# Optimization experiments

Measured on AMD Instinct MI355X. Metric: run time of the kernel, lower is better.

The kernel has to match this reference:

```python
import jax, jax.numpy as jnp
import numpy as np

B, Q, S1, S2 = 4, 256, 2048, 2048   # batch, latents, kv lengths
D, H, K, F = 2048, 16, 128, 8192    # embed_dim, heads, key_size, ffn dim
LN_EPS = 1e-5


def _layer_norm(x, scale, offset):
    mu = jnp.mean(x, axis=-1, keepdims=True)
    var = jnp.var(x, axis=-1, keepdims=True)
    return (x - mu) * jax.lax.rsqrt(var + LN_EPS) * scale + offset


def _cross_attention(q_in, kv_in, wq, bq, wk, bk, wv, bv, wo, bo, bias_k, bias_v):
    b, q_len, _ = q_in.shape
    t = kv_in.shape[1]
    qh = (q_in @ wq + bq).reshape(b, q_len, H, K)
    kh = (kv_in @ wk + bk).reshape(b, t, H, K)
    vh = (kv_in @ wv + bv).reshape(b, t, H, K)
    # ESM-style learned bias key/value appended as one extra kv position
    kh = jnp.concatenate([kh, jnp.broadcast_to(bias_k, (b, 1, H, K))], axis=1)
    vh = jnp.concatenate([vh, jnp.broadcast_to(bias_v, (b, 1, H, K))], axis=1)
    scale = jnp.sqrt(jnp.asarray(K, q_in.dtype))
    logits = jnp.einsum('bqhk,bthk->bhqt', qh, kh) / scale  # [B,H,Q,T+1]
    weights = jax.nn.softmax(logits, axis=-1)
    ctx = jnp.einsum('bhqt,bthk->bqhk', weights, vh).reshape(b, q_len, H * K)
    return ctx @ wo + bo


def _forward(x, xf_1, xf_2,
             ln1_scale, ln1_offset, wq1, bq1, wk1, bk1, wv1, bv1, wo1, bo1, bias_k1, bias_v1,
             ln2_scale, ln2_offset, wq2, bq2, wk2, bk2, wv2, bv2, wo2, bo2, bias_k2, bias_v2,
             ln_mlp_scale, ln_mlp_offset, w_fc1, b_fc1, w_fc2, b_fc2):
    res = x
    h = _layer_norm(x, ln1_scale, ln1_offset)
    x = res + _cross_attention(h, xf_1, wq1, bq1, wk1, bk1, wv1, bv1, wo1, bo1, bias_k1, bias_v1)
    res = x
    h = _layer_norm(x, ln2_scale, ln2_offset)
    x = res + _cross_attention(h, xf_2, wq2, bq2, wk2, bk2, wv2, bv2, wo2, bo2, bias_k2, bias_v2)
    h = _layer_norm(x, ln_mlp_scale, ln_mlp_offset)
    h = jax.nn.gelu(h @ w_fc1 + b_fc1, approximate=False) @ w_fc2 + b_fc2
    return x + h


def setup_inputs() -> dict:
    key = jax.random.key(0)
    ks = iter(jax.random.split(key, 64))

    def rn(shape, s=0.02):
        return jax.random.normal(next(ks), shape, jnp.float32) * s

    inp = {
        'x': rn((B, Q, D), 1.0),
        'xf_1': rn((B, S1, D), 1.0),
        'xf_2': rn((B, S2, D), 1.0),
    }
    for i in (1, 2):
        inp[f'ln{i}_scale'] = jnp.ones((D,), jnp.float32)
        inp[f'ln{i}_offset'] = jnp.zeros((D,), jnp.float32)
        inp[f'wq{i}'] = rn((D, H * K))
        inp[f'bq{i}'] = jnp.zeros((H * K,), jnp.float32)
        inp[f'wk{i}'] = rn((D, H * K))
        inp[f'bk{i}'] = jnp.zeros((H * K,), jnp.float32)
        inp[f'wv{i}'] = rn((D, H * K))
        inp[f'bv{i}'] = jnp.zeros((H * K,), jnp.float32)
        inp[f'wo{i}'] = rn((H * K, D))
        inp[f'bo{i}'] = jnp.zeros((D,), jnp.float32)
        inp[f'bias_k{i}'] = rn((1, 1, H, K))
        inp[f'bias_v{i}'] = rn((1, 1, H, K))
    inp['ln_mlp_scale'] = jnp.ones((D,), jnp.float32)
    inp['ln_mlp_offset'] = jnp.zeros((D,), jnp.float32)
    inp['w_fc1'] = rn((D, F))
    inp['b_fc1'] = jnp.zeros((F,), jnp.float32)
    inp['w_fc2'] = rn((F, D))
    inp['b_fc2'] = jnp.zeros((D,), jnp.float32)
    return inp


def reference(x, xf_1, xf_2,
              ln1_scale, ln1_offset, wq1, bq1, wk1, bk1, wv1, bv1, wo1, bo1, bias_k1, bias_v1,
              ln2_scale, ln2_offset, wq2, bq2, wk2, bk2, wv2, bv2, wo2, bo2, bias_k2, bias_v2,
              ln_mlp_scale, ln_mlp_offset, w_fc1, b_fc1, w_fc2, b_fc2):
    return _forward(x, xf_1, xf_2,
                    ln1_scale, ln1_offset, wq1, bq1, wk1, bk1, wv1, bv1, wo1, bo1, bias_k1, bias_v1,
                    ln2_scale, ln2_offset, wq2, bq2, wk2, bk2, wv2, bv2, wo2, bo2, bias_k2, bias_v2,
                    ln_mlp_scale, ln_mlp_offset, w_fc1, b_fc1, w_fc2, b_fc2)
```

## Files before the change

kernel.cpp:

```cpp
#include <hip/hip_runtime.h>

typedef __attribute__((ext_vector_type(8))) short bf16x8;
typedef __attribute__((ext_vector_type(4))) float f32x4;

#define D_EMB 2048
#define NQ    256
#define NB    4
#define NS    2048
#define NH    16
#define HK    128
#define FF    8192

__device__ __forceinline__ float b2f(short s) {
  union { unsigned int u; float f; } c;
  c.u = ((unsigned int)(unsigned short)s) << 16;
  return c.f;
}
__device__ __forceinline__ short f2b(float f) {
  union { float f; unsigned int u; } c; c.f = f;
  unsigned int u = c.u;
  u += 0x7FFFu + ((u >> 16) & 1u);
  return (short)(u >> 16);
}
__device__ __forceinline__ void gload_lds16(const short* g, short* l) {
  __builtin_amdgcn_global_load_lds(
      (const __attribute__((address_space(1))) void*)g,
      (__attribute__((address_space(3))) void*)l, 16, 0, 0);
}

__global__ __launch_bounds__(256)
void cvt_kernel(const float* __restrict__ in, short* __restrict__ out, int n8) {
  const int i = (blockIdx.x * 256 + threadIdx.x) * 8;
  if (i >= n8) return;
  f32x4 a = *(const f32x4*)(in + i), b = *(const f32x4*)(in + i + 4);
  bf16x8 t;
#pragma unroll
  for (int j = 0; j < 4; ++j) { t[j] = f2b(a[j]); t[4 + j] = f2b(b[j]); }
  *(bf16x8*)(out + i) = t;
}

__global__ __launch_bounds__(256)
void transpose_kernel(const float* __restrict__ W, short* __restrict__ Wt,
                      int Kd, int N) {
  __shared__ short tile[64][65];
  const int k0 = blockIdx.y * 64, n0 = blockIdx.x * 64;
  const int tid = threadIdx.x;
  const int r = tid >> 2, c4 = (tid & 3) * 16;
#pragma unroll
  for (int i = 0; i < 16; i += 4) {
    f32x4 v = *(const f32x4*)(W + (size_t)(k0 + r) * N + n0 + c4 + i);
#pragma unroll
    for (int j = 0; j < 4; ++j) tile[c4 + i + j][r] = f2b(v[j]);
  }
  __syncthreads();
  bf16x8 o0, o1;
#pragma unroll
  for (int j = 0; j < 8; ++j) { o0[j] = tile[r][c4 + j]; o1[j] = tile[r][c4 + 8 + j]; }
  short* dst = Wt + (size_t)(n0 + r) * Kd + k0 + c4;
  *(bf16x8*)dst = o0;
  *(bf16x8*)(dst + 8) = o1;
}

__global__ __launch_bounds__(256)
void ln_kernel(const float* __restrict__ x, const float* __restrict__ scale,
               const float* __restrict__ offset, short* __restrict__ out) {
  const int row = blockIdx.x, tid = threadIdx.x;
  const float* xr = x + (size_t)row * D_EMB + tid * 8;
  f32x4 v0 = *(const f32x4*)xr;
  f32x4 v1 = *(const f32x4*)(xr + 4);
  float f[8], s = 0.f, sq = 0.f;
#pragma unroll
  for (int i = 0; i < 4; ++i) { f[i] = v0[i]; f[4 + i] = v1[i]; }
#pragma unroll
  for (int i = 0; i < 8; ++i) { s += f[i]; sq += f[i] * f[i]; }
#pragma unroll
  for (int off = 1; off < 64; off <<= 1) {
    s  += __shfl_xor(s, off, 64);
    sq += __shfl_xor(sq, off, 64);
  }
  __shared__ float red[2][4];
  const int w = tid >> 6;
  if ((tid & 63) == 0) { red[0][w] = s; red[1][w] = sq; }
  __syncthreads();
  s  = red[0][0] + red[0][1] + red[0][2] + red[0][3];
  sq = red[1][0] + red[1][1] + red[1][2] + red[1][3];
  const float mu  = s * (1.f / D_EMB);
  const float var = sq * (1.f / D_EMB) - mu * mu;
  const float inv = rsqrtf(var + 1e-5f);
  bf16x8 ov;
#pragma unroll
  for (int i = 0; i < 8; ++i) {
    const int c = tid * 8 + i;
    ov[i] = f2b((f[i] - mu) * inv * scale[c] + offset[c]);
  }
  *(bf16x8*)(out + (size_t)row * D_EMB + tid * 8) = ov;
}

template<int EPI, int OUTF>
__global__ __launch_bounds__(256)
void gemm_kernel(const short* __restrict__ A, const short* __restrict__ Bt,
                 const float* __restrict__ bias, const float* __restrict__ res,
                 void* __restrict__ Cp, int M, int N, int Kd) {
  __shared__ short ldsA[128 * 32];
  __shared__ short ldsB[128 * 32];
  const int tid = threadIdx.x;
  const int m0 = blockIdx.y * 128, n0 = blockIdx.x * 128;
  const int w = tid >> 6, lane = tid & 63, l15 = lane & 15, quad = lane >> 4;
  const int wr = (w >> 1) * 64, wc = (w & 1) * 64;
  const int sr = tid >> 2;
  const int sc = (tid & 3) * 8;
  f32x4 acc[4][4];
#pragma unroll
  for (int mi = 0; mi < 4; ++mi)
#pragma unroll
    for (int ni = 0; ni < 4; ++ni) acc[mi][ni] = (f32x4){0.f, 0.f, 0.f, 0.f};

  const short* pa0 = A  + (size_t)(m0 + sr) * Kd + sc;
  const short* pa1 = A  + (size_t)(m0 + 64 + sr) * Kd + sc;
  const short* pb0 = Bt + (size_t)(n0 + sr) * Kd + sc;
  const short* pb1 = Bt + (size_t)(n0 + 64 + sr) * Kd + sc;

  for (int k0 = 0; k0 < Kd; k0 += 32) {
    __syncthreads();
    gload_lds16(pa0 + k0, ldsA + tid * 8);
    gload_lds16(pa1 + k0, ldsA + 2048 + tid * 8);
    gload_lds16(pb0 + k0, ldsB + tid * 8);
    gload_lds16(pb1 + k0, ldsB + 2048 + tid * 8);
    __syncthreads();
    bf16x8 af[4], bfr[4];
#pragma unroll
    for (int mi = 0; mi < 4; ++mi)
      af[mi] = *(bf16x8*)&ldsA[(wr + mi * 16 + l15) * 32 + quad * 8];
#pragma unroll
    for (int ni = 0; ni < 4; ++ni)
      bfr[ni] = *(bf16x8*)&ldsB[(wc + ni * 16 + l15) * 32 + quad * 8];
#pragma unroll
    for (int mi = 0; mi < 4; ++mi)
#pragma unroll
      for (int ni = 0; ni < 4; ++ni)
        acc[mi][ni] = __builtin_amdgcn_mfma_f32_16x16x32_bf16(
            af[mi], bfr[ni], acc[mi][ni], 0, 0, 0);
  }

#pragma unroll
  for (int mi = 0; mi < 4; ++mi) {
#pragma unroll
    for (int ni = 0; ni < 4; ++ni) {
      const int gn = n0 + wc + ni * 16 + l15;
      const float bv = bias[gn];
#pragma unroll
      for (int r = 0; r < 4; ++r) {
        const int gm = m0 + wr + mi * 16 + quad * 4 + r;
        float v = acc[mi][ni][r] + bv;
        if (EPI == 1) v += res[(size_t)gm * N + gn];
        if (EPI == 2) v = 0.5f * v * (1.f + erff(v * 0.70710678118654752f));
        if (OUTF) ((float*)Cp)[(size_t)gm * N + gn] = v;
        else      ((short*)Cp)[(size_t)gm * N + gn] = f2b(v);
      }
    }
  }
}

#define FENCE() asm volatile("" ::: "memory")

#define G_STAGE(DB2, DSTOFF, PS0, PS1, KON)                                     \
  gload_lds16((PS0) + (KON), sh + (DB2) * 32768 + (DSTOFF) + tid * 8);          \
  gload_lds16((PS1) + (KON), sh + (DB2) * 32768 + (DSTOFF) + 4096 + tid * 8);

#define PHASE(DB, MG, KH, DSTOFF, PS0, PS1, KON, DOVM)                          \
  {                                                                             \
    const short* _ra = sh + (DB) * 32768 + (KH) * 8192;                         \
    const short* _rb = sh + (DB) * 32768 + 16384 + (KH) * 8192;                 \
    if ((MG) == 0) {                                                            \
      bfrag[0] = *(const bf16x8*)(_rb + boff[0]);                               \
      bfrag[1] = *(const bf16x8*)(_rb + boff[1]);                               \
      bfrag[2] = *(const bf16x8*)(_rb + boff[2]);                               \
      bfrag[3] = *(const bf16x8*)(_rb + boff[3]);                               \
    }                                                                           \
    afrag[0] = *(const bf16x8*)(_ra + aoff[(MG) * 4 + 0]);                      \
    afrag[1] = *(const bf16x8*)(_ra + aoff[(MG) * 4 + 1]);                      \
    afrag[2] = *(const bf16x8*)(_ra + aoff[(MG) * 4 + 2]);                      \
    afrag[3] = *(const bf16x8*)(_ra + aoff[(MG) * 4 + 3]);                      \
    G_STAGE((DB) ^ 1, DSTOFF, PS0, PS1, KON)                                    \
    if (DOVM) asm volatile("s_waitcnt vmcnt(4)" ::: "memory");                  \
    __builtin_amdgcn_s_barrier();                                               \
    FENCE();                                                                    \
    __builtin_amdgcn_s_setprio(1);                                              \
    _Pragma("unroll")                                                           \
    for (int mf = 0; mf < 4; ++mf)                                              \
      _Pragma("unroll")                                                         \
      for (int nf = 0; nf < 4; ++nf)                                            \
        acc[(MG) * 4 + mf][nf] = __builtin_amdgcn_mfma_f32_16x16x32_bf16(       \
            afrag[mf], bfrag[nf], acc[(MG) * 4 + mf][nf], 0, 0, 0);             \
    __builtin_amdgcn_s_setprio(0);                                              \
    __builtin_amdgcn_s_barrier();                                               \
    FENCE();                                                                    \
  }

#define TILE(DB, KON)                                                           \
  PHASE(DB, 0, 0, 0,     pA0, pA1, (KON), 0)                                    \
  PHASE(DB, 1, 0, 16384, pB0, pB1, (KON), 1)                                    \
  PHASE(DB, 0, 1, 8192,  pA0, pA1, (KON) + 32, 0)                               \
  PHASE(DB, 1, 1, 24576, pB0, pB1, (KON) + 32, 1)

template<int EPI, int OUTF>
__global__ __launch_bounds__(512, 2)
void gemm256_kernel(const short* __restrict__ A, const short* __restrict__ Bt,
                    const float* __restrict__ bias, const float* __restrict__ res,
                    void* __restrict__ Cp, int M, int N, int Kd) {
  __shared__ short sh[65536];
  const int tid = threadIdx.x;
  const int w = tid >> 6, lane = tid & 63;
  const int l15 = lane & 15, quad = lane >> 4;
  const int wm = w >> 2, wn = w & 3;

  const int nTn = N >> 8;
  const int cpx = gridDim.x >> 3;
  const int wid = (blockIdx.x & 7) * cpx + (blockIdx.x >> 3);
  const int m0 = (wid / nTn) * 256, n0 = (wid % nTn) * 256;

  const int c0 = tid, c1 = 512 + tid;
  const int r0 = ((c0 >> 5) << 3) + (c0 & 7), kb0 = (c0 >> 3) & 3;
  const int r1 = ((c1 >> 5) << 3) + (c1 & 7), kb1 = (c1 >> 3) & 3;
  const short* pA0 = A  + (size_t)(m0 + r0) * Kd + kb0 * 8;
  const short* pA1 = A  + (size_t)(m0 + r1) * Kd + kb1 * 8;
  const short* pB0 = Bt + (size_t)(n0 + r0) * Kd + kb0 * 8;
  const short* pB1 = Bt + (size_t)(n0 + r1) * Kd + kb1 * 8;

  int aoff[8], boff[4];
#pragma unroll
  for (int mf = 0; mf < 8; ++mf) {
    const int r = wm * 128 + mf * 16 + l15;
    aoff[mf] = ((r >> 3) << 8) + (quad << 6) + ((r & 7) << 3);
  }
#pragma unroll
  for (int nf = 0; nf < 4; ++nf) {
    const int r = wn * 64 + nf * 16 + l15;
    boff[nf] = ((r >> 3) << 8) + (quad << 6) + ((r & 7) << 3);
  }

  f32x4 acc[8][4];
#pragma unroll
  for (int mf = 0; mf < 8; ++mf)
#pragma unroll
    for (int nf = 0; nf < 4; ++nf) acc[mf][nf] = (f32x4){0.f, 0.f, 0.f, 0.f};
  bf16x8 afrag[4], bfrag[4];

  const int NT = Kd >> 6;

  G_STAGE(0, 0,     pA0, pA1, 0)
  G_STAGE(0, 16384, pB0, pB1, 0)
  G_STAGE(0, 8192,  pA0, pA1, 32)
  G_STAGE(0, 24576, pB0, pB1, 32)
  asm volatile("s_waitcnt vmcnt(4)" ::: "memory");
  __builtin_amdgcn_s_barrier();
  FENCE();

  for (int kt = 0; kt < NT; kt += 2) {
    const int k1n = (kt + 1) * 64;
    const int k2n = (kt + 2 < NT) ? (kt + 2) * 64 : 0;
    TILE(0, k1n)
    TILE(1, k2n)
  }
  asm volatile("s_waitcnt vmcnt(0) lgkmcnt(0)" ::: "memory");

#pragma unroll
  for (int mf = 0; mf < 8; ++mf) {
#pragma unroll
    for (int nf = 0; nf < 4; ++nf) {
      const int gn = n0 + wn * 64 + nf * 16 + l15;
      const float bv = bias[gn];
#pragma unroll
      for (int r = 0; r < 4; ++r) {
        const int gm = m0 + wm * 128 + mf * 16 + quad * 4 + r;
        float v = acc[mf][nf][r] + bv;
        if (EPI == 1) v += res[(size_t)gm * N + gn];
        if (EPI == 2) v = 0.5f * v * (1.f + erff(v * 0.70710678118654752f));
        if (OUTF) ((float*)Cp)[(size_t)gm * N + gn] = v;
        else      ((short*)Cp)[(size_t)gm * N + gn] = f2b(v);
      }
    }
  }
}

__global__ __launch_bounds__(256)
void attn_part_kernel(const short* __restrict__ qh, const short* __restrict__ kh,
                      const short* __restrict__ vh, float* __restrict__ po,
                      float* __restrict__ pml) {
  const int bx = blockIdx.x;
  const int work = (bx & 7) * 128 + (bx >> 3);
  const int bh = work >> 4, sub = work & 15;
  const int qt = sub >> 2, split = sub & 3;
  const int b = bh >> 4, h = bh & 15;
  const int tid = threadIdx.x, w = tid >> 6, lane = tid & 63;
  const int l15 = lane & 15, quad = lane >> 4;
  const int q0 = qt * 64 + w * 16;

  __shared__ short ldsK[32 * 128];
  __shared__ short ldsV[128 * 32];
  __shared__ short ldsP[4 * 16 * 32];

  const float sc = 0.08838834764831845f;

  bf16x8 aq[4];
  {
    const short* qrow = qh + ((size_t)(b * 256 + q0 + l15)) * D_EMB + h * 128;
#pragma unroll
    for (int s = 0; s < 4; ++s)
      aq[s] = *(const bf16x8*)(qrow + s * 32 + quad * 8);
  }

  f32x4 o[8];
  float m_run[4], l_run[4];
#pragma unroll
  for (int dt = 0; dt < 8; ++dt) o[dt] = (f32x4){0.f, 0.f, 0.f, 0.f};
#pragma unroll
  for (int r = 0; r < 4; ++r) { m_run[r] = -INFINITY; l_run[r] = 0.f; }

  const int srow = tid >> 4;
  const int j = tid & 15;
  const int ksw = (j ^ (srow & 7)) * 8;
  const int t_beg = split * 512;

  for (int t0 = t_beg; t0 < t_beg + 512; t0 += 32) {
    __syncthreads();
    const size_t kb0 = ((size_t)(b * NS + t0 + srow)) * D_EMB + h * 128;
    const size_t kb1 = kb0 + (size_t)16 * D_EMB;
    gload_lds16(kh + kb0 + ksw, ldsK + tid * 8);
    gload_lds16(kh + kb1 + ksw, ldsK + 2048 + tid * 8);
    {
      bf16x8 v0 = *(const bf16x8*)(vh + kb0 + j * 8);
      bf16x8 v1 = *(const bf16x8*)(vh + kb1 + j * 8);
#pragma unroll
      for (int i = 0; i < 8; ++i) {
        const int d = j * 8 + i;
        const int swz = ((d >> 3) & 3) << 4;
        char* base = (char*)ldsV + (d << 6);
        *(short*)(base + ((srow << 1) ^ swz))        = v0[i];
        *(short*)(base + (((srow + 16) << 1) ^ swz)) = v1[i];
      }
    }
    __syncthreads();

    f32x4 s0 = (f32x4){0.f, 0.f, 0.f, 0.f}, s1 = (f32x4){0.f, 0.f, 0.f, 0.f};
    const int kswr = (l15 & 7) << 4;
#pragma unroll
    for (int s = 0; s < 4; ++s) {
      const int cb = s * 64 + quad * 16;
      bf16x8 k0f = *(bf16x8*)((char*)ldsK + (l15 << 8)        + (cb ^ kswr));
      bf16x8 k1f = *(bf16x8*)((char*)ldsK + ((16 + l15) << 8) + (cb ^ kswr));
      s0 = __builtin_amdgcn_mfma_f32_16x16x32_bf16(aq[s], k0f, s0, 0, 0, 0);
      s1 = __builtin_amdgcn_mfma_f32_16x16x32_bf16(aq[s], k1f, s1, 0, 0, 0);
    }

    float alpha_r[4];
#pragma unroll
    for (int r = 0; r < 4; ++r) {
      const float v0 = s0[r] * sc, v1 = s1[r] * sc;
      float mx = fmaxf(v0, v1);
#pragma unroll
      for (int off = 1; off < 16; off <<= 1) mx = fmaxf(mx, __shfl_xor(mx, off, 16));
      const float m_new = fmaxf(m_run[r], mx);
      const float p0 = expf(v0 - m_new), p1 = expf(v1 - m_new);
      float rs = p0 + p1;
#pragma unroll
      for (int off = 1; off < 16; off <<= 1) rs += __shfl_xor(rs, off, 16);
      alpha_r[r] = expf(m_run[r] - m_new);
      l_run[r] = l_run[r] * alpha_r[r] + rs;
      m_run[r] = m_new;
      const int prow = quad * 4 + r;
      const int psw = ((prow >> 1) & 3) << 4;
      char* pb = (char*)ldsP + w * 1024 + (prow << 6);
      *(short*)(pb + ((l15 << 1) ^ psw))        = f2b(p0);
      *(short*)(pb + (((16 + l15) << 1) ^ psw)) = f2b(p1);
    }
#pragma unroll
    for (int dt = 0; dt < 8; ++dt)
#pragma unroll
      for (int r = 0; r < 4; ++r) o[dt][r] *= alpha_r[r];

    bf16x8 pf = *(bf16x8*)((char*)ldsP + w * 1024 + (l15 << 6) +
                           ((quad << 4) ^ (((l15 >> 1) & 3) << 4)));
#pragma unroll
    for (int dt = 0; dt < 8; ++dt) {
      const int drow = dt * 16 + l15;
      bf16x8 vf = *(bf16x8*)((char*)ldsV + (drow << 6) +
                             ((quad << 4) ^ (((drow >> 3) & 3) << 4)));
      o[dt] = __builtin_amdgcn_mfma_f32_16x16x32_bf16(pf, vf, o[dt], 0, 0, 0);
    }
  }

  const int orow_base = (bh * 4 + qt) * 64 + w * 16;
#pragma unroll
  for (int dt = 0; dt < 8; ++dt)
#pragma unroll
    for (int r = 0; r < 4; ++r) {
      const size_t orow = (size_t)(orow_base + quad * 4 + r);
      po[(orow * 4 + split) * 128 + dt * 16 + l15] = o[dt][r];
    }
  if (l15 == 0) {
#pragma unroll
    for (int r = 0; r < 4; ++r) {
      const size_t orow = (size_t)(orow_base + quad * 4 + r);
      pml[(orow * 4 + split) * 2]     = m_run[r];
      pml[(orow * 4 + split) * 2 + 1] = l_run[r];
    }
  }
}

__global__ __launch_bounds__(256)
void attn_combine_kernel(const short* __restrict__ qh, const float* __restrict__ bias_k,
                         const float* __restrict__ bias_v, const float* __restrict__ po,
                         const float* __restrict__ pml, short* __restrict__ ctx) {
  const int tid = threadIdx.x, w = tid >> 6, lane = tid & 63;
  const int task = blockIdx.x * 4 + w;
  const int bh = task >> 8, qr = task & 255;
  const int b = bh >> 4, h = bh & 15;
  const int d0 = lane * 2;
  const float sc = 0.08838834764831845f;

  const short* qrow = qh + ((size_t)(b * 256 + qr)) * D_EMB + h * 128 + d0;
  const unsigned int qv = *(const unsigned int*)qrow;
  const float q0 = b2f((short)(qv & 0xffffu));
  const float q1 = b2f((short)(qv >> 16));
  const float2 bk = *(const float2*)(bias_k + h * 128 + d0);
  float le = q0 * bk.x + q1 * bk.y;
#pragma unroll
  for (int off = 1; off < 64; off <<= 1) le += __shfl_xor(le, off, 64);
  le *= sc;

  const float* pm = pml + (size_t)task * 8;
  float m[4], l[4];
#pragma unroll
  for (int s = 0; s < 4; ++s) { m[s] = pm[s * 2]; l[s] = pm[s * 2 + 1]; }
  float mt = le;
#pragma unroll
  for (int s = 0; s < 4; ++s) mt = fmaxf(mt, m[s]);

  const float pe = expf(le - mt);
  const float2 bv = *(const float2*)(bias_v + h * 128 + d0);
  float acc0 = pe * bv.x, acc1 = pe * bv.y;
  float lt = pe;
#pragma unroll
  for (int s = 0; s < 4; ++s) {
    const float es = expf(m[s] - mt);
    lt += l[s] * es;
    const float2 op = *(const float2*)(po + ((size_t)task * 4 + s) * 128 + d0);
    acc0 += es * op.x;
    acc1 += es * op.y;
  }
  const float inv = 1.f / lt;
  const unsigned int pack =
      ((unsigned int)(unsigned short)f2b(acc1 * inv) << 16) |
      (unsigned short)f2b(acc0 * inv);
  *(unsigned int*)(ctx + ((size_t)(b * 256 + qr)) * D_EMB + h * 128 + d0) = pack;
}

extern "C" void kernel_launch(void* const* d_in, const int* in_sizes, int n_in,
                              void* d_out, int out_size, void* d_ws, size_t ws_size,
                              hipStream_t stream) {
  const float* x   = (const float*)d_in[0];
  const float* xf1 = (const float*)d_in[1];
  const float* xf2 = (const float*)d_in[2];
  const float* L1[12]; const float* L2[12];
  for (int j = 0; j < 12; ++j) { L1[j] = (const float*)d_in[3 + j]; L2[j] = (const float*)d_in[15 + j]; }
  const float* ln_mlp_s = (const float*)d_in[27];
  const float* ln_mlp_o = (const float*)d_in[28];
  const float* w_fc1    = (const float*)d_in[29];
  const float* b_fc1    = (const float*)d_in[30];
  const float* w_fc2    = (const float*)d_in[31];
  const float* b_fc2    = (const float*)d_in[32];
  float* out = (float*)d_out;

  const size_t SZ_XQ  = (size_t)NB * NQ * D_EMB;
  const size_t SZ_KV  = (size_t)NB * NS * D_EMB;
  const size_t SZ_W   = (size_t)FF * D_EMB;

  float* x1   = (float*)d_ws;
  float* x2   = x1 + SZ_XQ;
  short* h_ln = (short*)(x2 + SZ_XQ);
  short* qh   = h_ln + SZ_XQ;
  short* ctxb = qh + SZ_XQ;
  short* kh   = ctxb + SZ_XQ;
  short* vh   = kh + SZ_KV;
  short* xfb  = vh + SZ_KV;
  short* Wt   = xfb + SZ_KV;
  short* fc1b = kh;
  float* po   = (float*)Wt;
  float* pml  = (float*)h_ln;

  const dim3 blk(256);
  const dim3 blk5(512);
  const dim3 g_q(D_EMB / 128, (NB * NQ) / 128);
  const dim3 g_kv256((NB * NS / 256) * (D_EMB / 256));
  const dim3 g_f1(FF / 128, (NB * NQ) / 128);
  const dim3 g_tw(D_EMB / 64, D_EMB / 64);
  const dim3 g_tf1(FF / 64, D_EMB / 64);
  const dim3 g_tf2(D_EMB / 64, FF / 64);
  const int  g_cvt = (int)(SZ_KV / 8 / 256);

  cvt_kernel<<<g_cvt, blk, 0, stream>>>(xf1, xfb, (int)SZ_KV);
  ln_kernel<<<NB * NQ, blk, 0, stream>>>(x, L1[0], L1[1], h_ln);
  transpose_kernel<<<g_tw, blk, 0, stream>>>(L1[2], Wt, D_EMB, D_EMB);
  gemm_kernel<0,0><<<g_q,  blk, 0, stream>>>(h_ln, Wt, L1[3], nullptr, qh, NB * NQ, D_EMB, D_EMB);
  transpose_kernel<<<g_tw, blk, 0, stream>>>(L1[4], Wt, D_EMB, D_EMB);
  gemm256_kernel<0,0><<<g_kv256, blk5, 0, stream>>>(xfb, Wt, L1[5], nullptr, kh, NB * NS, D_EMB, D_EMB);
  transpose_kernel<<<g_tw, blk, 0, stream>>>(L1[6], Wt, D_EMB, D_EMB);
  gemm256_kernel<0,0><<<g_kv256, blk5, 0, stream>>>(xfb, Wt, L1[7], nullptr, vh, NB * NS, D_EMB, D_EMB);
  attn_part_kernel<<<1024, blk, 0, stream>>>(qh, kh, vh, po, pml);
  attn_combine_kernel<<<4096, blk, 0, stream>>>(qh, L1[10], L1[11], po, pml, ctxb);
  transpose_kernel<<<g_tw, blk, 0, stream>>>(L1[8], Wt, D_EMB, D_EMB);
  gemm_kernel<1,1><<<g_q,  blk, 0, stream>>>(ctxb, Wt, L1[9], x, x1, NB * NQ, D_EMB, D_EMB);

  cvt_kernel<<<g_cvt, blk, 0, stream>>>(xf2, xfb, (int)SZ_KV);
  ln_kernel<<<NB * NQ, blk, 0, stream>>>(x1, L2[0], L2[1], h_ln);
  transpose_kernel<<<g_tw, blk, 0, stream>>>(L2[2], Wt, D_EMB, D_EMB);
  gemm_kernel<0,0><<<g_q,  blk, 0, stream>>>(h_ln, Wt, L2[3], nullptr, qh, NB * NQ, D_EMB, D_EMB);
  transpose_kernel<<<g_tw, blk, 0, stream>>>(L2[4], Wt, D_EMB, D_EMB);
  gemm256_kernel<0,0><<<g_kv256, blk5, 0, stream>>>(xfb, Wt, L2[5], nullptr, kh, NB * NS, D_EMB, D_EMB);
  transpose_kernel<<<g_tw, blk, 0, stream>>>(L2[6], Wt, D_EMB, D_EMB);
  gemm256_kernel<0,0><<<g_kv256, blk5, 0, stream>>>(xfb, Wt, L2[7], nullptr, vh, NB * NS, D_EMB, D_EMB);
  attn_part_kernel<<<1024, blk, 0, stream>>>(qh, kh, vh, po, pml);
  attn_combine_kernel<<<4096, blk, 0, stream>>>(qh, L2[10], L2[11], po, pml, ctxb);
  transpose_kernel<<<g_tw, blk, 0, stream>>>(L2[8], Wt, D_EMB, D_EMB);
  gemm_kernel<1,1><<<g_q,  blk, 0, stream>>>(ctxb, Wt, L2[9], x1, x2, NB * NQ, D_EMB, D_EMB);

  ln_kernel<<<NB * NQ, blk, 0, stream>>>(x2, ln_mlp_s, ln_mlp_o, h_ln);
  transpose_kernel<<<g_tf1, blk, 0, stream>>>(w_fc1, Wt, D_EMB, FF);
  gemm_kernel<2,0><<<g_f1, blk, 0, stream>>>(h_ln, Wt, b_fc1, nullptr, fc1b, NB * NQ, FF, D_EMB);
  transpose_kernel<<<g_tf2, blk, 0, stream>>>(w_fc2, Wt, FF, D_EMB);
  gemm_kernel<1,1><<<g_q,  blk, 0, stream>>>(fc1b, Wt, b_fc2, x2, out, NB * NQ, D_EMB, FF);
}
```

Measured before the change: 1.299 ms.

## Replace small-M GEMMs with split-K 256-tile kernel plus combine epilogue

Adds a split-K mode to the 256x256 pipelined GEMM kernel. It is used for the Q, output and FC projections, where M=1024 gave the old 128-tile kernel too few blocks to fill the GPU. Each split writes fp32 partials into reused workspace (the K/V buffers). A new vectorized combine kernel then sums the partials and applies bias, residual or GELU. The trade is more CU parallelism and a stronger inner loop against large extra partial-sum traffic (tens of MB per GEMM) and one extra launch per GEMM.

```diff
diff --git a/kernel.cpp b/kernel.cpp
--- a/kernel.cpp
+++ b/kernel.cpp
@@ -1,6 +1,7 @@
 #include <hip/hip_runtime.h>
 
 typedef __attribute__((ext_vector_type(8))) short bf16x8;
+typedef __attribute__((ext_vector_type(4))) short short4v;
 typedef __attribute__((ext_vector_type(4))) float f32x4;
 
 #define D_EMB 2048
@@ -94,71 +95,6 @@
     ov[i] = f2b((f[i] - mu) * inv * scale[c] + offset[c]);
   }
   *(bf16x8*)(out + (size_t)row * D_EMB + tid * 8) = ov;
-}
-
-template<int EPI, int OUTF>
-__global__ __launch_bounds__(256)
-void gemm_kernel(const short* __restrict__ A, const short* __restrict__ Bt,
-                 const float* __restrict__ bias, const float* __restrict__ res,
-                 void* __restrict__ Cp, int M, int N, int Kd) {
-  __shared__ short ldsA[128 * 32];
-  __shared__ short ldsB[128 * 32];
-  const int tid = threadIdx.x;
-  const int m0 = blockIdx.y * 128, n0 = blockIdx.x * 128;
-  const int w = tid >> 6, lane = tid & 63, l15 = lane & 15, quad = lane >> 4;
-  const int wr = (w >> 1) * 64, wc = (w & 1) * 64;
-  const int sr = tid >> 2;
-  const int sc = (tid & 3) * 8;
-  f32x4 acc[4][4];
-#pragma unroll
-  for (int mi = 0; mi < 4; ++mi)
-#pragma unroll
-    for (int ni = 0; ni < 4; ++ni) acc[mi][ni] = (f32x4){0.f, 0.f, 0.f, 0.f};
-
-  const short* pa0 = A  + (size_t)(m0 + sr) * Kd + sc;
-  const short* pa1 = A  + (size_t)(m0 + 64 + sr) * Kd + sc;
-  const short* pb0 = Bt + (size_t)(n0 + sr) * Kd + sc;
-  const short* pb1 = Bt + (size_t)(n0 + 64 + sr) * Kd + sc;
-
-  for (int k0 = 0; k0 < Kd; k0 += 32) {
-    __syncthreads();
-    gload_lds16(pa0 + k0, ldsA + tid * 8);
-    gload_lds16(pa1 + k0, ldsA + 2048 + tid * 8);
-    gload_lds16(pb0 + k0, ldsB + tid * 8);
-    gload_lds16(pb1 + k0, ldsB + 2048 + tid * 8);
-    __syncthreads();
-    bf16x8 af[4], bfr[4];
-#pragma unroll
-    for (int mi = 0; mi < 4; ++mi)
-      af[mi] = *(bf16x8*)&ldsA[(wr + mi * 16 + l15) * 32 + quad * 8];
-#pragma unroll
-    for (int ni = 0; ni < 4; ++ni)
-      bfr[ni] = *(bf16x8*)&ldsB[(wc + ni * 16 + l15) * 32 + quad * 8];
-#pragma unroll
-    for (int mi = 0; mi < 4; ++mi)
-#pragma unroll
-      for (int ni = 0; ni < 4; ++ni)
-        acc[mi][ni] = __builtin_amdgcn_mfma_f32_16x16x32_bf16(
-            af[mi], bfr[ni], acc[mi][ni], 0, 0, 0);
-  }
-
-#pragma unroll
-  for (int mi = 0; mi < 4; ++mi) {
-#pragma unroll
-    for (int ni = 0; ni < 4; ++ni) {
-      const int gn = n0 + wc + ni * 16 + l15;
-      const float bv = bias[gn];
-#pragma unroll
-      for (int r = 0; r < 4; ++r) {
-        const int gm = m0 + wr + mi * 16 + quad * 4 + r;
-        float v = acc[mi][ni][r] + bv;
-        if (EPI == 1) v += res[(size_t)gm * N + gn];
-        if (EPI == 2) v = 0.5f * v * (1.f + erff(v * 0.70710678118654752f));
-        if (OUTF) ((float*)Cp)[(size_t)gm * N + gn] = v;
-        else      ((short*)Cp)[(size_t)gm * N + gn] = f2b(v);
-      }
-    }
-  }
 }
 
 #define FENCE() asm volatile("" ::: "memory")
@@ -203,7 +139,7 @@
   PHASE(DB, 0, 1, 8192,  pA0, pA1, (KON) + 32, 0)                               \
   PHASE(DB, 1, 1, 24576, pB0, pB1, (KON) + 32, 1)
 
-template<int EPI, int OUTF>
+template<int EPI, int OUTF, int SPLITK>
 __global__ __launch_bounds__(512, 2)
 void gemm256_kernel(const short* __restrict__ A, const short* __restrict__ Bt,
                     const float* __restrict__ bias, const float* __restrict__ res,
@@ -215,9 +151,14 @@
   const int wm = w >> 2, wn = w & 3;
 
   const int nTn = N >> 8;
+  const int ntiles = (M >> 8) * nTn;
   const int cpx = gridDim.x >> 3;
   const int wid = (blockIdx.x & 7) * cpx + (blockIdx.x >> 3);
-  const int m0 = (wid / nTn) * 256, n0 = (wid % nTn) * 256;
+  const int tile  = (SPLITK == 1) ? wid : (wid % ntiles);
+  const int split = (SPLITK == 1) ? 0   : (wid / ntiles);
+  const int Ko = Kd / SPLITK;
+  const int ks = split * Ko;
+  const int m0 = (tile / nTn) * 256, n0 = (tile % nTn) * 256;
 
   const int c0 = tid, c1 = 512 + tid;
   const int r0 = ((c0 >> 5) << 3) + (c0 & 7), kb0 = (c0 >> 3) & 3;
@@ -246,40 +187,94 @@
     for (int nf = 0; nf < 4; ++nf) acc[mf][nf] = (f32x4){0.f, 0.f, 0.f, 0.f};
   bf16x8 afrag[4], bfrag[4];
 
-  const int NT = Kd >> 6;
-
-  G_STAGE(0, 0,     pA0, pA1, 0)
-  G_STAGE(0, 16384, pB0, pB1, 0)
-  G_STAGE(0, 8192,  pA0, pA1, 32)
-  G_STAGE(0, 24576, pB0, pB1, 32)
+  const int NT = Ko >> 6;
+
+  G_STAGE(0, 0,     pA0, pA1, ks)
+  G_STAGE(0, 16384, pB0, pB1, ks)
+  G_STAGE(0, 8192,  pA0, pA1, ks + 32)
+  G_STAGE(0, 24576, pB0, pB1, ks + 32)
   asm volatile("s_waitcnt vmcnt(4)" ::: "memory");
   __builtin_amdgcn_s_barrier();
   FENCE();
 
   for (int kt = 0; kt < NT; kt += 2) {
-    const int k1n = (kt + 1) * 64;
-    const int k2n = (kt + 2 < NT) ? (kt + 2) * 64 : 0;
+    const int k1n = ks + (kt + 1) * 64;
+    const int k2n = (kt + 2 < NT) ? ks + (kt + 2) * 64 : ks;
     TILE(0, k1n)
     TILE(1, k2n)
   }
   asm volatile("s_waitcnt vmcnt(0) lgkmcnt(0)" ::: "memory");
 
-#pragma unroll
-  for (int mf = 0; mf < 8; ++mf) {
-#pragma unroll
-    for (int nf = 0; nf < 4; ++nf) {
-      const int gn = n0 + wn * 64 + nf * 16 + l15;
-      const float bv = bias[gn];
-#pragma unroll
-      for (int r = 0; r < 4; ++r) {
-        const int gm = m0 + wm * 128 + mf * 16 + quad * 4 + r;
-        float v = acc[mf][nf][r] + bv;
-        if (EPI == 1) v += res[(size_t)gm * N + gn];
-        if (EPI == 2) v = 0.5f * v * (1.f + erff(v * 0.70710678118654752f));
-        if (OUTF) ((float*)Cp)[(size_t)gm * N + gn] = v;
-        else      ((short*)Cp)[(size_t)gm * N + gn] = f2b(v);
+  if (SPLITK == 1) {
+#pragma unroll
+    for (int mf = 0; mf < 8; ++mf) {
+#pragma unroll
+      for (int nf = 0; nf < 4; ++nf) {
+        const int gn = n0 + wn * 64 + nf * 16 + l15;
+        const float bv = bias[gn];
+#pragma unroll
+        for (int r = 0; r < 4; ++r) {
+          const int gm = m0 + wm * 128 + mf * 16 + quad * 4 + r;
+          float v = acc[mf][nf][r] + bv;
+          if (EPI == 1) v += res[(size_t)gm * N + gn];
+          if (EPI == 2) v = 0.5f * v * (1.f + erff(v * 0.70710678118654752f));
+          if (OUTF) ((float*)Cp)[(size_t)gm * N + gn] = v;
+          else      ((short*)Cp)[(size_t)gm * N + gn] = f2b(v);
+        }
       }
     }
+  } else {
+    float* po = (float*)Cp + (size_t)split * M * N;
+#pragma unroll
+    for (int mf = 0; mf < 8; ++mf) {
+#pragma unroll
+      for (int nf = 0; nf < 4; ++nf) {
+        const int gn = n0 + wn * 64 + nf * 16 + l15;
+#pragma unroll
+        for (int r = 0; r < 4; ++r) {
+          const int gm = m0 + wm * 128 + mf * 16 + quad * 4 + r;
+          po[(size_t)gm * N + gn] = acc[mf][nf][r];
+        }
+      }
+    }
+  }
+}
+
+template<int S, int EPI, int OUTF>
+__global__ __launch_bounds__(256)
+void combine_kernel(const float* __restrict__ po, const float* __restrict__ bias,
+                    const float* __restrict__ res, void* __restrict__ out,
+                    int M, int N) {
+  const size_t i4 = ((size_t)blockIdx.x * 256 + threadIdx.x) * 4;
+  if (i4 >= (size_t)M * N) return;
+  const int n = (int)(i4 % N);
+  f32x4 s = *(const f32x4*)(po + i4);
+#pragma unroll
+  for (int sp = 1; sp < S; ++sp) {
+    const f32x4 p = *(const f32x4*)(po + (size_t)sp * M * N + i4);
+#pragma unroll
+    for (int j = 0; j < 4; ++j) s[j] += p[j];
+  }
+  const f32x4 bv = *(const f32x4*)(bias + n);
+#pragma unroll
+  for (int j = 0; j < 4; ++j) s[j] += bv[j];
+  if (EPI == 1) {
+    const f32x4 rv = *(const f32x4*)(res + i4);
+#pragma unroll
+    for (int j = 0; j < 4; ++j) s[j] += rv[j];
+  }
+  if (EPI == 2) {
+#pragma unroll
+    for (int j = 0; j < 4; ++j)
+      s[j] = 0.5f * s[j] * (1.f + erff(s[j] * 0.70710678118654752f));
+  }
+  if (OUTF) {
+    *(f32x4*)((float*)out + i4) = s;
+  } else {
+    short4v o;
+#pragma unroll
+    for (int j = 0; j < 4; ++j) o[j] = f2b(s[j]);
+    *(short4v*)((short*)out + i4) = o;
   }
 }
 
@@ -474,7 +469,6 @@
 
   const size_t SZ_XQ  = (size_t)NB * NQ * D_EMB;
   const size_t SZ_KV  = (size_t)NB * NS * D_EMB;
-  const size_t SZ_W   = (size_t)FF * D_EMB;
 
   float* x1   = (float*)d_ws;
   float* x2   = x1 + SZ_XQ;
@@ -488,12 +482,16 @@
   short* fc1b = kh;
   float* po   = (float*)Wt;
   float* pml  = (float*)h_ln;
+  float* pk1  = (float*)kh;
+  float* pk2  = (float*)vh;
 
   const dim3 blk(256);
   const dim3 blk5(512);
-  const dim3 g_q(D_EMB / 128, (NB * NQ) / 128);
   const dim3 g_kv256((NB * NS / 256) * (D_EMB / 256));
-  const dim3 g_f1(FF / 128, (NB * NQ) / 128);
+  const dim3 g_sk(256);
+  const dim3 g_skf1(256);
+  const dim3 g_cb2(2048);
+  const dim3 g_cb8(8192);
   const dim3 g_tw(D_EMB / 64, D_EMB / 64);
   const dim3 g_tf1(FF / 64, D_EMB / 64);
   const dim3 g_tf2(D_EMB / 64, FF / 64);
@@ -502,32 +500,38 @@
   cvt_kernel<<<g_cvt, blk, 0, stream>>>(xf1, xfb, (int)SZ_KV);
   ln_kernel<<<NB * NQ, blk, 0, stream>>>(x, L1[0], L1[1], h_ln);
   transpose_kernel<<<g_tw, blk, 0, stream>>>(L1[2], Wt, D_EMB, D_EMB);
-  gemm_kernel<0,0><<<g_q,  blk, 0, stream>>>(h_ln, Wt, L1[3], nullptr, qh, NB * NQ, D_EMB, D_EMB);
+  gemm256_kernel<0,0,8><<<g_sk, blk5, 0, stream>>>(h_ln, Wt, nullptr, nullptr, pk1, NB * NQ, D_EMB, D_EMB);
+  combine_kernel<8,0,0><<<g_cb2, blk, 0, stream>>>(pk1, L1[3], nullptr, qh, NB * NQ, D_EMB);
   transpose_kernel<<<g_tw, blk, 0, stream>>>(L1[4], Wt, D_EMB, D_EMB);
-  gemm256_kernel<0,0><<<g_kv256, blk5, 0, stream>>>(xfb, Wt, L1[5], nullptr, kh, NB * NS, D_EMB, D_EMB);
+  gemm256_kernel<0,0,1><<<g_kv256, blk5, 0, stream>>>(xfb, Wt, L1[5], nullptr, kh, NB * NS, D_EMB, D_EMB);
   transpose_kernel<<<g_tw, blk, 0, stream>>>(L1[6], Wt, D_EMB, D_EMB);
-  gemm256_kernel<0,0><<<g_kv256, blk5, 0, stream>>>(xfb, Wt, L1[7], nullptr, vh, NB * NS, D_EMB, D_EMB);
+  gemm256_kernel<0,0,1><<<g_kv256, blk5, 0, stream>>>(xfb, Wt, L1[7], nullptr, vh, NB * NS, D_EMB, D_EMB);
   attn_part_kernel<<<1024, blk, 0, stream>>>(qh, kh, vh, po, pml);
   attn_combine_kernel<<<4096, blk, 0, stream>>>(qh, L1[10], L1[11], po, pml, ctxb);
   transpose_kernel<<<g_tw, blk, 0, stream>>>(L1[8], Wt, D_EMB, D_EMB);
-  gemm_kernel<1,1><<<g_q,  blk, 0, stream>>>(ctxb, Wt, L1[9], x, x1, NB * NQ, D_EMB, D_EMB);
+  gemm256_kernel<0,0,8><<<g_sk, blk5, 0, stream>>>(ctxb, Wt, nullptr, nullptr, pk1, NB * NQ, D_EMB, D_EMB);
+  combine_kernel<8,1,1><<<g_cb2, blk, 0, stream>>>(pk1, L1[9], x, x1, NB * NQ, D_EMB);
 
   cvt_kernel<<<g_cvt, blk, 0, stream>>>(xf2, xfb, (int)SZ_KV);
   ln_kernel<<<NB * NQ, blk, 0, stream>>>(x1, L2[0], L2[1], h_ln);
   transpose_kernel<<<g_tw, blk, 0, stream>>>(L2[2], Wt, D_EMB, D_EMB);
-  gemm_kernel<0,0><<<g_q,  blk, 0, stream>>>(h_ln, Wt, L2[3], nullptr, qh, NB * NQ, D_EMB, D_EMB);
+  gemm256_kernel<0,0,8><<<g_sk, blk5, 0, stream>>>(h_ln, Wt, nullptr, nullptr, pk1, NB * NQ, D_EMB, D_EMB);
+  combine_kernel<8,0,0><<<g_cb2, blk, 0, stream>>>(pk1, L2[3], nullptr, qh, NB * NQ, D_EMB);
   transpose_kernel<<<g_tw, blk, 0, stream>>>(L2[4], Wt, D_EMB, D_EMB);
-  gemm256_kernel<0,0><<<g_kv256, blk5, 0, stream>>>(xfb, Wt, L2[5], nullptr, kh, NB * NS, D_EMB, D_EMB);
+  gemm256_kernel<0,0,1><<<g_kv256, blk5, 0, stream>>>(xfb, Wt, L2[5], nullptr, kh, NB * NS, D_EMB, D_EMB);
   transpose_kernel<<<g_tw, blk, 0, stream>>>(L2[6], Wt, D_EMB, D_EMB);
-  gemm256_kernel<0,0><<<g_kv256, blk5, 0, stream>>>(xfb, Wt, L2[7], nullptr, vh, NB * NS, D_EMB, D_EMB);
+  gemm256_kernel<0,0,1><<<g_kv256, blk5, 0, stream>>>(xfb, Wt, L2[7], nullptr, vh, NB * NS, D_EMB, D_EMB);
   attn_part_kernel<<<1024, blk, 0, stream>>>(qh, kh, vh, po, pml);
   attn_combine_kernel<<<4096, blk, 0, stream>>>(qh, L2[10], L2[11], po, pml, ctxb);
   transpose_kernel<<<g_tw, blk, 0, stream>>>(L2[8], Wt, D_EMB, D_EMB);
-  gemm_kernel<1,1><<<g_q,  blk, 0, stream>>>(ctxb, Wt, L2[9], x1, x2, NB * NQ, D_EMB, D_EMB);
+  gemm256_kernel<0,0,8><<<g_sk, blk5, 0, stream>>>(ctxb, Wt, nullptr, nullptr, pk1, NB * NQ, D_EMB, D_EMB);
+  combine_kernel<8,1,1><<<g_cb2, blk, 0, stream>>>(pk1, L2[9], x1, x2, NB * NQ, D_EMB);
 
   ln_kernel<<<NB * NQ, blk, 0, stream>>>(x2, ln_mlp_s, ln_mlp_o, h_ln);
   transpose_kernel<<<g_tf1, blk, 0, stream>>>(w_fc1, Wt, D_EMB, FF);
-  gemm_kernel<2,0><<<g_f1, blk, 0, stream>>>(h_ln, Wt, b_fc1, nullptr, fc1b, NB * NQ, FF, D_EMB);
+  gemm256_kernel<0,0,2><<<g_skf1, blk5, 0, stream>>>(h_ln, Wt, nullptr, nullptr, pk2, NB * NQ, FF, D_EMB);
+  combine_kernel<2,2,0><<<g_cb8, blk, 0, stream>>>(pk2, b_fc1, nullptr, fc1b, NB * NQ, FF);
   transpose_kernel<<<g_tf2, blk, 0, stream>>>(w_fc2, Wt, FF, D_EMB);
-  gemm_kernel<1,1><<<g_q,  blk, 0, stream>>>(fc1b, Wt, b_fc2, x2, out, NB * NQ, D_EMB, FF);
-}
+  gemm256_kernel<0,0,8><<<g_sk, blk5, 0, stream>>>(fc1b, Wt, nullptr, nullptr, pk2, NB * NQ, D_EMB, FF);
+  combine_kernel<8,1,1><<<g_cb2, blk, 0, stream>>>(pk2, b_fc2, x2, out, NB * NQ, D_EMB);
+}
```

After: 1.173 ms. -9.7%, faster.
